# Optimization experiments

Hardware: AMD Instinct MI355X
Metric: run time of the kernel (lower is better)

## Reference

```python
import jax, jax.numpy as jnp
import numpy as np

N, E = 40000, 640000
EMB, HID, H, TXT = 128, 128, 4, 384
C = HID // H  # per-head channels = 32


def _prelu(x, a):
    return jnp.where(x >= 0, x, a * x)


def _layernorm(x, g, b, eps=1e-5):
    m = jnp.mean(x, axis=-1, keepdims=True)
    v = jnp.mean((x - m) ** 2, axis=-1, keepdims=True)
    return (x - m) / jnp.sqrt(v + eps) * g + b


def _gat_conv(h, src, dst, W, att_src, att_dst, bias):
    # PyG GATConv (concat=True, eval mode): lin has no bias, self-loops already in src/dst.
    xh = (h @ W.T).reshape(N, H, C)                      # [N,H,C]
    a_src = jnp.sum(xh * att_src, axis=-1)               # [N,H]
    a_dst = jnp.sum(xh * att_dst, axis=-1)               # [N,H]
    alpha = jax.nn.leaky_relu(a_src[src] + a_dst[dst], negative_slope=0.2)  # [Et,H]
    amax = jax.ops.segment_max(alpha, dst, num_segments=N)
    ex = jnp.exp(alpha - amax[dst])
    denom = jax.ops.segment_sum(ex, dst, num_segments=N)
    coef = ex / denom[dst]                               # scatter-softmax over dst
    out = jax.ops.segment_sum(xh[src] * coef[:, :, None], dst, num_segments=N)
    return out.reshape(N, H * C) + bias


def setup_inputs() -> dict:
    key = jax.random.key(0)
    ks = jax.random.split(key, 20)
    nrm = lambda k, s, sc=0.05: jax.random.normal(k, s, jnp.float32) * sc
    inp = {
        "x": nrm(ks[0], (N, EMB), 1.0),
        "num_x": nrm(ks[1], (N, 1), 1.0),
        "num_mask": jnp.ones((N,), jnp.float32),
        "txt_x": nrm(ks[2], (N, TXT), 1.0),
        "txt_mask": jnp.ones((N,), jnp.float32),
        "edge_index": jax.random.randint(ks[3], (2, E), 0, N, jnp.int32),
        "num_proj_w": nrm(ks[4], (EMB, 1)), "num_proj_b": jnp.zeros((EMB,), jnp.float32),
        "txt_proj_w": nrm(ks[5], (EMB, TXT)), "txt_proj_b": jnp.zeros((EMB,), jnp.float32),
        "node_proj_w": nrm(ks[6], (HID, EMB)), "node_proj_b": jnp.zeros((HID,), jnp.float32),
        "prelu0_a": jnp.full((HID,), 0.25, jnp.float32),
        "conv1_w": nrm(ks[7], (HID, HID)), "att_src1": nrm(ks[8], (H, C)), "att_dst1": nrm(ks[9], (H, C)), "bias1": jnp.zeros((HID,), jnp.float32),
        "norm1_g": jnp.ones((HID,), jnp.float32), "norm1_b": jnp.zeros((HID,), jnp.float32),
        "prelu1_a": jnp.full((HID,), 0.25, jnp.float32),
        "conv2_w": nrm(ks[10], (HID, HID)), "att_src2": nrm(ks[11], (H, C)), "att_dst2": nrm(ks[12], (H, C)), "bias2": jnp.zeros((HID,), jnp.float32),
        "norm2_g": jnp.ones((HID,), jnp.float32), "norm2_b": jnp.zeros((HID,), jnp.float32),
        "prelu2_a": jnp.full((HID,), 0.25, jnp.float32),
        "out_w": nrm(ks[13], (1, HID)), "out_b": jnp.zeros((1,), jnp.float32),
    }
    return inp


def reference(x, num_x, num_mask, txt_x, txt_mask, edge_index,
              num_proj_w, num_proj_b, txt_proj_w, txt_proj_b,
              node_proj_w, node_proj_b, prelu0_a,
              conv1_w, att_src1, att_dst1, bias1, norm1_g, norm1_b, prelu1_a,
              conv2_w, att_src2, att_dst2, bias2, norm2_g, norm2_b, prelu2_a,
              out_w, out_b):
    # add self loops (PyG GATConv default)
    loop = jnp.arange(N, dtype=edge_index.dtype)
    src = jnp.concatenate([edge_index[0], loop])
    dst = jnp.concatenate([edge_index[1], loop])

    h = (num_x * num_mask[:, None]) @ num_proj_w.T + num_proj_b
    h = h + (txt_x * txt_mask[:, None]) @ txt_proj_w.T + txt_proj_b
    h = h + x @ node_proj_w.T + node_proj_b
    h = _prelu(h, prelu0_a)

    h = _gat_conv(h, src, dst, conv1_w, att_src1, att_dst1, bias1)
    h = _prelu(_layernorm(h, norm1_g, norm1_b), prelu1_a)  # dropout: eval mode -> identity

    h = _gat_conv(h, src, dst, conv2_w, att_src2, att_dst2, bias2)
    h = _prelu(_layernorm(h, norm2_g, norm2_b), prelu2_a)

    return (h @ out_w.T + out_b).squeeze(-1)  # [N]
```

## Files before the change

### kernel.cpp

```cpp
#include <hip/hip_runtime.h>
#include <stdint.h>

typedef unsigned short u16;
typedef unsigned int u32;
typedef __attribute__((ext_vector_type(8))) short bf16x8;
typedef __attribute__((ext_vector_type(4))) float f32x4;

__device__ __forceinline__ float bf2f(u32 u) {
    union { u32 i; float f; } v; v.i = u << 16; return v.f;
}
__device__ __forceinline__ u16 f2bf(float f) {
    u32 x = __float_as_uint(f);
    return (u16)((x + 0x7fffu + ((x >> 16) & 1u)) >> 16);
}
__device__ __forceinline__ float wred_sum(float v) {
#pragma unroll
    for (int o = 32; o > 0; o >>= 1) v += __shfl_xor(v, o, 64);
    return v;
}
__device__ __forceinline__ bf16x8 ldA_f32(const float* p, size_t off) {
    union { uint4 u; bf16x8 b; } t;
    const float* af = p + off;
    float4 a = *(const float4*)af, b2 = *(const float4*)(af + 4);
    t.u.x = (u32)f2bf(a.x)  | ((u32)f2bf(a.y)  << 16);
    t.u.y = (u32)f2bf(a.z)  | ((u32)f2bf(a.w)  << 16);
    t.u.z = (u32)f2bf(b2.x) | ((u32)f2bf(b2.y) << 16);
    t.u.w = (u32)f2bf(b2.z) | ((u32)f2bf(b2.w) << 16);
    return t.b;
}
__device__ __forceinline__ bf16x8 ld16B(const u16* p, size_t off) {
    union { uint4 u; bf16x8 b; } t; t.u = *(const uint4*)(p + off); return t.b;
}
__device__ __forceinline__ bf16x8 ldB(const u16* sw, int ct, int ks, int l16, int quad) {
    union { uint4 u; bf16x8 b; } t;
    t.u = *(const uint4*)&sw[(ct * 16 + l16) * 136 + ks * 32 + quad * 8];
    return t.b;
}
__device__ __forceinline__ void stage256_f32(const float* W, int stride, int koff,
                                             u16* sw, int tid) {
#pragma unroll
    for (int it = 0; it < 8; ++it) {
        int idx = (it * 256 + tid) * 8;
        int c = idx >> 7, kk = idx & 127;
        const float* wf = W + (size_t)c * stride + koff + kk;
        float4 a = *(const float4*)wf, b = *(const float4*)(wf + 4);
        uint4 v;
        v.x = (u32)f2bf(a.x) | ((u32)f2bf(a.y) << 16);
        v.y = (u32)f2bf(a.z) | ((u32)f2bf(a.w) << 16);
        v.z = (u32)f2bf(b.x) | ((u32)f2bf(b.y) << 16);
        v.w = (u32)f2bf(b.z) | ((u32)f2bf(b.w) << 16);
        *(uint4*)&sw[c * 136 + kk] = v;
    }
}

__global__ void k_zero(int* __restrict__ p, int n) {
    int i = blockIdx.x * 256 + threadIdx.x;
    if (i < n) p[i] = 0;
}
__global__ void k_hist(const int* __restrict__ dst, int E, int* __restrict__ deg) {
    int e = blockIdx.x * 256 + threadIdx.x;
    if (e < E) atomicAdd(&deg[dst[e]], 1);
}
__global__ __launch_bounds__(1024) void k_scanA(const int* __restrict__ deg, int n,
                                                int* __restrict__ out, int* __restrict__ bsum) {
    __shared__ int wsum[16];
    int t = threadIdx.x, w = t >> 6, lane = t & 63;
    int i0 = blockIdx.x * 4096 + t * 4;
    int4 v = make_int4(0, 0, 0, 0);
    if (i0 + 3 < n) v = *(const int4*)&deg[i0];
    else {
        if (i0 < n)     v.x = deg[i0];
        if (i0 + 1 < n) v.y = deg[i0 + 1];
        if (i0 + 2 < n) v.z = deg[i0 + 2];
    }
    int tsum = v.x + v.y + v.z + v.w;
    int s = tsum;
#pragma unroll
    for (int o = 1; o < 64; o <<= 1) { int u = __shfl_up(s, o, 64); if (lane >= o) s += u; }
    if (lane == 63) wsum[w] = s;
    __syncthreads();
    if (w == 0 && lane < 16) {
        int ws = wsum[lane];
#pragma unroll
        for (int o = 1; o < 16; o <<= 1) { int u = __shfl_up(ws, o, 64); if (lane >= o) ws += u; }
        wsum[lane] = ws;
    }
    __syncthreads();
    int woff = (w == 0) ? 0 : wsum[w - 1];
    int p = woff + s - tsum;
    if (i0 + 3 < n) {
        int4 o4; o4.x = p; o4.y = p + v.x; o4.z = p + v.x + v.y; o4.w = p + v.x + v.y + v.z;
        *(int4*)&out[i0] = o4;
    } else {
        int pp = p;
        if (i0 < n)     { out[i0] = pp;     pp += v.x; }
        if (i0 + 1 < n) { out[i0 + 1] = pp; pp += v.y; }
        if (i0 + 2 < n) { out[i0 + 2] = pp; }
    }
    if (t == 0) bsum[blockIdx.x] = wsum[15];
}
__global__ void k_scanB(int* __restrict__ bsum, int nb, int* __restrict__ total) {
    int lane = threadIdx.x;
    int v = (lane < nb) ? bsum[lane] : 0;
    int s = v;
#pragma unroll
    for (int o = 1; o < 64; o <<= 1) { int u = __shfl_up(s, o, 64); if (lane >= o) s += u; }
    if (lane < nb) bsum[lane] = s - v;
    if (lane == 63) total[0] = s;
}
__global__ void k_scanC(int* __restrict__ rowptr, int* __restrict__ cursor,
                        const int* __restrict__ boff, int n) {
    int i = blockIdx.x * 256 + threadIdx.x;
    if (i < n) {
        int r = rowptr[i] + boff[i >> 12];
        rowptr[i] = r; cursor[i] = r;
    }
}
__global__ void k_scatter(const int* __restrict__ srcp, const int* __restrict__ dstp, int E,
                          int* __restrict__ cursor, int* __restrict__ col) {
    int e = blockIdx.x * 256 + threadIdx.x;
    if (e < E) {
        int p = atomicAdd(&cursor[dstp[e]], 1);
        col[p] = srcp[e];
    }
}

__global__ __launch_bounds__(256) void k_fused1(
    const float* __restrict__ x, const float* __restrict__ numx, const float* __restrict__ numm,
    const float* __restrict__ txt, const float* __restrict__ txtm,
    const float* __restrict__ numw, const float* __restrict__ numb,
    const float* __restrict__ txtw, const float* __restrict__ txtb,
    const float* __restrict__ nodew, const float* __restrict__ nodeb,
    const float* __restrict__ pa,
    const float* __restrict__ W1, const float* __restrict__ atts, const float* __restrict__ attd,
    u16* __restrict__ xh, float* __restrict__ asrc, float* __restrict__ adst) {
    __shared__ u16 sw[128 * 136];
    __shared__ u16 sh[4][16 * 136];
    int tid = threadIdx.x, w = tid >> 6, lane = tid & 63, quad = lane >> 4, l16 = lane & 15;
    int nb = blockIdx.x * 64 + w * 16;
    f32x4 acc[8];
#pragma unroll
    for (int ct = 0; ct < 8; ++ct) { f32x4 z = {0.f, 0.f, 0.f, 0.f}; acc[ct] = z; }

    for (int chunk = 0; chunk < 3; ++chunk) {
        __syncthreads();
        stage256_f32(txtw, 384, chunk * 128, sw, tid);
        __syncthreads();
#pragma unroll
        for (int ks = 0; ks < 4; ++ks) {
            bf16x8 a0 = ldA_f32(txt, (size_t)(nb + l16) * 384 + chunk * 128 + ks * 32 + quad * 8);
#pragma unroll
            for (int ct = 0; ct < 8; ++ct)
                acc[ct] = __builtin_amdgcn_mfma_f32_16x16x32_bf16(
                    a0, ldB(sw, ct, ks, l16, quad), acc[ct], 0, 0, 0);
        }
    }
#pragma unroll
    for (int r = 0; r < 4; ++r) {
        float tm = txtm[nb + quad * 4 + r];
#pragma unroll
        for (int ct = 0; ct < 8; ++ct) acc[ct][r] *= tm;
    }
    __syncthreads();
    stage256_f32(nodew, 128, 0, sw, tid);
    __syncthreads();
#pragma unroll
    for (int ks = 0; ks < 4; ++ks) {
        bf16x8 a0 = ldA_f32(x, (size_t)(nb + l16) * 128 + ks * 32 + quad * 8);
#pragma unroll
        for (int ct = 0; ct < 8; ++ct)
            acc[ct] = __builtin_amdgcn_mfma_f32_16x16x32_bf16(
                a0, ldB(sw, ct, ks, l16, quad), acc[ct], 0, 0, 0);
    }
    float nm[4];
#pragma unroll
    for (int r = 0; r < 4; ++r) {
        int n = nb + quad * 4 + r;
        nm[r] = numx[n] * numm[n];
    }
#pragma unroll
    for (int ct = 0; ct < 8; ++ct) {
        int c = ct * 16 + l16;
        float cw = numw[c];
        float cb = numb[c] + txtb[c] + nodeb[c];
        float pav = pa[c];
#pragma unroll
        for (int r = 0; r < 4; ++r) {
            float v = acc[ct][r] + nm[r] * cw + cb;
            v = v >= 0.f ? v : pav * v;
            sh[w][(quad * 4 + r) * 136 + c] = f2bf(v);
        }
    }
    __syncthreads();
    stage256_f32(W1, 128, 0, sw, tid);
    __syncthreads();
    f32x4 a2[8];
#pragma unroll
    for (int ct = 0; ct < 8; ++ct) { f32x4 z = {0.f, 0.f, 0.f, 0.f}; a2[ct] = z; }
#pragma unroll
    for (int ks = 0; ks < 4; ++ks) {
        bf16x8 a0 = ld16B(sh[w], l16 * 136 + ks * 32 + quad * 8);
#pragma unroll
        for (int ct = 0; ct < 8; ++ct)
            a2[ct] = __builtin_amdgcn_mfma_f32_16x16x32_bf16(
                a0, ldB(sw, ct, ks, l16, quad), a2[ct], 0, 0, 0);
    }
#pragma unroll
    for (int ct = 0; ct < 8; ++ct) {
        int c = ct * 16 + l16;
#pragma unroll
        for (int r = 0; r < 4; ++r)
            xh[(size_t)(nb + quad * 4 + r) * 128 + c] = f2bf(a2[ct][r]);
    }
    float as_[8], ad_[8];
#pragma unroll
    for (int ct = 0; ct < 8; ++ct) {
        int c = ct * 16 + l16;
        as_[ct] = atts[c];
        ad_[ct] = attd[c];
    }
#pragma unroll
    for (int hh = 0; hh < 4; ++hh) {
        float vs[4], vd[4];
#pragma unroll
        for (int r = 0; r < 4; ++r) {
            vs[r] = a2[2 * hh][r] * as_[2 * hh] + a2[2 * hh + 1][r] * as_[2 * hh + 1];
            vd[r] = a2[2 * hh][r] * ad_[2 * hh] + a2[2 * hh + 1][r] * ad_[2 * hh + 1];
        }
#pragma unroll
        for (int o = 1; o <= 8; o <<= 1) {
#pragma unroll
            for (int r = 0; r < 4; ++r) {
                vs[r] += __shfl_xor(vs[r], o, 64);
                vd[r] += __shfl_xor(vd[r], o, 64);
            }
        }
        if ((l16 >> 2) == hh) {
            int r = l16 & 3;
            float ss = (r == 0) ? vs[0] : (r == 1) ? vs[1] : (r == 2) ? vs[2] : vs[3];
            float dd = (r == 0) ? vd[0] : (r == 1) ? vd[1] : (r == 2) ? vd[2] : vd[3];
            int n = nb + quad * 4 + r;
            asrc[n * 4 + hh] = ss;
            adst[n * 4 + hh] = dd;
        }
    }
}

__global__ __launch_bounds__(256) void k_xh(
    const u16* __restrict__ h, const float* __restrict__ W,
    const float* __restrict__ att_s, const float* __restrict__ att_d,
    u16* __restrict__ xh, float* __restrict__ asrc, float* __restrict__ adst) {
    __shared__ u16 sw[128 * 136];
    int tid = threadIdx.x;
    int w = tid >> 6, lane = tid & 63, quad = lane >> 4, l16 = lane & 15;
    int nb = blockIdx.x * 64 + w * 16;
    f32x4 acc[8];
#pragma unroll
    for (int ct = 0; ct < 8; ++ct) { f32x4 z = {0.f, 0.f, 0.f, 0.f}; acc[ct] = z; }

    stage256_f32(W, 128, 0, sw, tid);
    __syncthreads();
#pragma unroll
    for (int ks = 0; ks < 4; ++ks) {
        bf16x8 a0 = ld16B(h, (size_t)(nb + l16) * 128 + ks * 32 + quad * 8);
#pragma unroll
        for (int ct = 0; ct < 8; ++ct)
            acc[ct] = __builtin_amdgcn_mfma_f32_16x16x32_bf16(
                a0, ldB(sw, ct, ks, l16, quad), acc[ct], 0, 0, 0);
    }
#pragma unroll
    for (int ct = 0; ct < 8; ++ct) {
        int c = ct * 16 + l16;
#pragma unroll
        for (int r = 0; r < 4; ++r) {
            int n = nb + quad * 4 + r;
            xh[(size_t)n * 128 + c] = f2bf(acc[ct][r]);
        }
    }
    float as_[8], ad_[8];
#pragma unroll
    for (int ct = 0; ct < 8; ++ct) {
        int c = ct * 16 + l16;
        as_[ct] = att_s[c];
        ad_[ct] = att_d[c];
    }
#pragma unroll
    for (int hh = 0; hh < 4; ++hh) {
        float vs[4], vd[4];
#pragma unroll
        for (int r = 0; r < 4; ++r) {
            vs[r] = acc[2 * hh][r] * as_[2 * hh] + acc[2 * hh + 1][r] * as_[2 * hh + 1];
            vd[r] = acc[2 * hh][r] * ad_[2 * hh] + acc[2 * hh + 1][r] * ad_[2 * hh + 1];
        }
#pragma unroll
        for (int o = 1; o <= 8; o <<= 1) {
#pragma unroll
            for (int r = 0; r < 4; ++r) {
                vs[r] += __shfl_xor(vs[r], o, 64);
                vd[r] += __shfl_xor(vd[r], o, 64);
            }
        }
        if ((l16 >> 2) == hh) {
            int r = l16 & 3;
            float ss = (r == 0) ? vs[0] : (r == 1) ? vs[1] : (r == 2) ? vs[2] : vs[3];
            float dd = (r == 0) ? vd[0] : (r == 1) ? vd[1] : (r == 2) ? vd[2] : vd[3];
            int n = nb + quad * 4 + r;
            asrc[n * 4 + hh] = ss;
            adst[n * 4 + hh] = dd;
        }
    }
}

__global__ __launch_bounds__(64) void k_agg(
    const u16* __restrict__ xh, const float* __restrict__ asrc, const float* __restrict__ adst,
    const int* __restrict__ rowptr, const int* __restrict__ col,
    const float* __restrict__ bias, const float* __restrict__ g, const float* __restrict__ b,
    const float* __restrict__ pa, u16* __restrict__ hnext,
    const float* __restrict__ outw, const float* __restrict__ outb, float* __restrict__ outy,
    int is_final) {
    __shared__ int   scol[64];
    __shared__ float scoef[64][4];
    int n = blockIdx.x, lane = threadIdx.x;
    int beg = rowptr[n], end = rowptr[n + 1];
    const float4* asrc4 = (const float4*)asrc;

    float4 adv = ((const float4*)adst)[n];
    float ad[4] = { adv.x, adv.y, adv.z, adv.w };
    float4 asv = asrc4[n];
    float els[4];
#pragma unroll
    for (int h = 0; h < 4; h++) {
        float a = ((const float*)&asv)[h] + ad[h];
        a = a >= 0.f ? a : 0.2f * a;
        els[h] = __expf(a);
    }
    int hh = lane >> 4;
    u32 vself = ((const u32*)(xh + (size_t)n * 128))[lane];
    float acc0 = els[hh] * bf2f(vself & 0xffffu);
    float acc1 = els[hh] * bf2f(vself >> 16);
    float a0b = 0.f, a1b = 0.f, a0c = 0.f, a1c = 0.f, a0d = 0.f, a1d = 0.f;
    float l[4] = { 0.f, 0.f, 0.f, 0.f };

    for (int base = beg; base < end; base += 64) {
        int e = base + lane;
        int cnt = min(64, end - base);
        if (e < end) {
            int s = col[e];
            float4 av = asrc4[s];
            scol[lane] = s;
            float cf[4];
#pragma unroll
            for (int h = 0; h < 4; h++) {
                float a = ((const float*)&av)[h] + ad[h];
                a = a >= 0.f ? a : 0.2f * a;
                cf[h] = __expf(a);
                l[h] += cf[h];
            }
            *(float4*)scoef[lane] = make_float4(cf[0], cf[1], cf[2], cf[3]);
        }
        __syncthreads();
        int j = 0;
        for (; j + 3 < cnt; j += 4) {
            int s0 = scol[j], s1 = scol[j + 1], s2 = scol[j + 2], s3 = scol[j + 3];
            float c0 = scoef[j][hh], c1 = scoef[j + 1][hh];
            float c2 = scoef[j + 2][hh], c3 = scoef[j + 3][hh];
            u32 v0 = ((const u32*)(xh + (size_t)s0 * 128))[lane];
            u32 v1 = ((const u32*)(xh + (size_t)s1 * 128))[lane];
            u32 v2 = ((const u32*)(xh + (size_t)s2 * 128))[lane];
            u32 v3 = ((const u32*)(xh + (size_t)s3 * 128))[lane];
            acc0 += c0 * bf2f(v0 & 0xffffu);  acc1 += c0 * bf2f(v0 >> 16);
            a0b  += c1 * bf2f(v1 & 0xffffu);  a1b  += c1 * bf2f(v1 >> 16);
            a0c  += c2 * bf2f(v2 & 0xffffu);  a1c  += c2 * bf2f(v2 >> 16);
            a0d  += c3 * bf2f(v3 & 0xffffu);  a1d  += c3 * bf2f(v3 >> 16);
        }
        for (; j < cnt; ++j) {
            int s0 = scol[j];
            float c0 = scoef[j][hh];
            u32 v0 = ((const u32*)(xh + (size_t)s0 * 128))[lane];
            acc0 += c0 * bf2f(v0 & 0xffffu);
            acc1 += c0 * bf2f(v0 >> 16);
        }
        __syncthreads();
    }
    acc0 += a0b + a0c + a0d;
    acc1 += a1b + a1c + a1d;

    float L[4];
#pragma unroll
    for (int h = 0; h < 4; h++) L[h] = wred_sum(l[h]) + els[h];
    float inv = 1.f / L[hh];
    acc0 *= inv;
    acc1 *= inv;

    int c0i = 2 * lane;
    float2 bi = *(const float2*)(bias + c0i);
    acc0 += bi.x; acc1 += bi.y;

    float mean = wred_sum(acc0 + acc1) * (1.f / 128.f);
    float d0 = acc0 - mean, d1 = acc1 - mean;
    float var = wred_sum(d0 * d0 + d1 * d1) * (1.f / 128.f);
    float rstd = rsqrtf(var + 1e-5f);
    float2 gg = *(const float2*)(g + c0i);
    float2 bb = *(const float2*)(b + c0i);
    float2 pp = *(const float2*)(pa + c0i);
    float y0 = d0 * rstd * gg.x + bb.x;
    float y1 = d1 * rstd * gg.y + bb.y;
    y0 = y0 >= 0.f ? y0 : pp.x * y0;
    y1 = y1 >= 0.f ? y1 : pp.y * y1;

    if (is_final) {
        float2 ow = *(const float2*)(outw + c0i);
        float dot = wred_sum(y0 * ow.x + y1 * ow.y);
        if (lane == 0) outy[n] = dot + outb[0];
    } else {
        ((u32*)(hnext + (size_t)n * 128))[lane] = (u32)f2bf(y0) | ((u32)f2bf(y1) << 16);
    }
}

extern "C" void kernel_launch(void* const* d_in, const int* in_sizes, int n_in,
                              void* d_out, int out_size, void* d_ws, size_t ws_size,
                              hipStream_t stream) {
    const int N = in_sizes[2];
    const int E = in_sizes[5] / 2;

    const float* x      = (const float*)d_in[0];
    const float* numx   = (const float*)d_in[1];
    const float* numm   = (const float*)d_in[2];
    const float* txt    = (const float*)d_in[3];
    const float* txtm   = (const float*)d_in[4];
    const int*   ei     = (const int*)d_in[5];
    const float* numw   = (const float*)d_in[6];
    const float* numb   = (const float*)d_in[7];
    const float* txtw   = (const float*)d_in[8];
    const float* txtb   = (const float*)d_in[9];
    const float* nodew  = (const float*)d_in[10];
    const float* nodeb  = (const float*)d_in[11];
    const float* pa0    = (const float*)d_in[12];
    const float* conv1w = (const float*)d_in[13];
    const float* atts1  = (const float*)d_in[14];
    const float* attd1  = (const float*)d_in[15];
    const float* bias1  = (const float*)d_in[16];
    const float* g1     = (const float*)d_in[17];
    const float* b1     = (const float*)d_in[18];
    const float* pa1    = (const float*)d_in[19];
    const float* conv2w = (const float*)d_in[20];
    const float* atts2  = (const float*)d_in[21];
    const float* attd2  = (const float*)d_in[22];
    const float* bias2  = (const float*)d_in[23];
    const float* g2     = (const float*)d_in[24];
    const float* b2     = (const float*)d_in[25];
    const float* pa2    = (const float*)d_in[26];
    const float* outw   = (const float*)d_in[27];
    const float* outb   = (const float*)d_in[28];

    const int* srcp = ei;
    const int* dstp = ei + E;

    char* p = (char*)d_ws;
    auto alloc = [&](size_t bytes) -> void* {
        void* q = (void*)p;
        p += (bytes + 255) & ~(size_t)255;
        return q;
    };
    u16*   hA     = (u16*)alloc((size_t)N * 128 * 2);
    u16*   hB     = (u16*)alloc((size_t)N * 128 * 2);
    float* asrc   = (float*)alloc((size_t)N * 4 * 4);
    float* adst   = (float*)alloc((size_t)N * 4 * 4);
    int*   deg    = (int*)alloc((size_t)N * 4);
    int*   rowptr = (int*)alloc((size_t)(N + 1) * 4);
    int*   cursor = (int*)alloc((size_t)N * 4);
    int*   col    = (int*)alloc((size_t)E * 4);
    int*   bsum   = (int*)alloc(64 * 4);

    const int nbScan = (N + 4095) / 4096;
    k_zero<<<(N + 255) / 256, 256, 0, stream>>>(deg, N);
    k_hist<<<(E + 255) / 256, 256, 0, stream>>>(dstp, E, deg);
    k_scanA<<<nbScan, 1024, 0, stream>>>(deg, N, rowptr, bsum);
    k_scanB<<<1, 64, 0, stream>>>(bsum, nbScan, rowptr + N);
    k_scanC<<<(N + 255) / 256, 256, 0, stream>>>(rowptr, cursor, bsum, N);
    k_scatter<<<(E + 255) / 256, 256, 0, stream>>>(srcp, dstp, E, cursor, col);

    const int gProj = N / 64;

    k_fused1<<<gProj, 256, 0, stream>>>(x, numx, numm, txt, txtm, numw, numb,
                                        txtw, txtb, nodew, nodeb, pa0,
                                        conv1w, atts1, attd1, hB, asrc, adst);
    k_agg<<<N, 64, 0, stream>>>(hB, asrc, adst, rowptr, col, bias1, g1, b1, pa1,
                                hA, nullptr, nullptr, nullptr, 0);

    k_xh<<<gProj, 256, 0, stream>>>(hA, conv2w, atts2, attd2, hB, asrc, adst);
    k_agg<<<N, 64, 0, stream>>>(hB, asrc, adst, rowptr, col, bias2, g2, b2, pa2,
                                nullptr, outw, outb, (float*)d_out, 1);
}
```

Before: 330.4 us.

## Pack four nodes per aggregation block, unroll gathers by eight, vectorize CSR build

The aggregation kernel now processes four destination nodes per 256-thread block, one wavefront each, with per-wave shared buffers. This removes the block-wide barriers, since each wave only reads its own staging area. The gather loop is unrolled to eight outstanding row loads to raise memory-level parallelism. Histogram and scatter kernels now read four edge indices per thread with int4 loads, which cuts the thread count. Dropping the barriers relies on wave-level execution ordering for the shared-memory writes and reads, with no explicit fence.

Measured after the change: 331.8 us. Within noise of the previous version (+0.4%).

```diff
diff --git a/kernel.cpp b/kernel.cpp
--- a/kernel.cpp
+++ b/kernel.cpp
@@ -58,8 +58,16 @@
     if (i < n) p[i] = 0;
 }
 __global__ void k_hist(const int* __restrict__ dst, int E, int* __restrict__ deg) {
-    int e = blockIdx.x * 256 + threadIdx.x;
-    if (e < E) atomicAdd(&deg[dst[e]], 1);
+    int i0 = (blockIdx.x * 256 + threadIdx.x) * 4;
+    if (i0 + 3 < E) {
+        int4 d = *(const int4*)&dst[i0];
+        atomicAdd(&deg[d.x], 1);
+        atomicAdd(&deg[d.y], 1);
+        atomicAdd(&deg[d.z], 1);
+        atomicAdd(&deg[d.w], 1);
+    } else {
+        for (int e = i0; e < E; ++e) atomicAdd(&deg[dst[e]], 1);
+    }
 }
 __global__ __launch_bounds__(1024) void k_scanA(const int* __restrict__ deg, int n,
                                                 int* __restrict__ out, int* __restrict__ bsum) {
@@ -118,10 +126,17 @@
 }
 __global__ void k_scatter(const int* __restrict__ srcp, const int* __restrict__ dstp, int E,
                           int* __restrict__ cursor, int* __restrict__ col) {
-    int e = blockIdx.x * 256 + threadIdx.x;
-    if (e < E) {
-        int p = atomicAdd(&cursor[dstp[e]], 1);
-        col[p] = srcp[e];
+    int i0 = (blockIdx.x * 256 + threadIdx.x) * 4;
+    if (i0 + 3 < E) {
+        int4 s = *(const int4*)&srcp[i0];
+        int4 d = *(const int4*)&dstp[i0];
+        col[atomicAdd(&cursor[d.x], 1)] = s.x;
+        col[atomicAdd(&cursor[d.y], 1)] = s.y;
+        col[atomicAdd(&cursor[d.z], 1)] = s.z;
+        col[atomicAdd(&cursor[d.w], 1)] = s.w;
+    } else {
+        for (int e = i0; e < E; ++e)
+            col[atomicAdd(&cursor[dstp[e]], 1)] = srcp[e];
     }
 }
 
@@ -311,16 +326,18 @@
     }
 }
 
-__global__ __launch_bounds__(64) void k_agg(
+__global__ __launch_bounds__(256) void k_agg(
     const u16* __restrict__ xh, const float* __restrict__ asrc, const float* __restrict__ adst,
     const int* __restrict__ rowptr, const int* __restrict__ col,
     const float* __restrict__ bias, const float* __restrict__ g, const float* __restrict__ b,
     const float* __restrict__ pa, u16* __restrict__ hnext,
     const float* __restrict__ outw, const float* __restrict__ outb, float* __restrict__ outy,
-    int is_final) {
-    __shared__ int   scol[64];
-    __shared__ float scoef[64][4];
-    int n = blockIdx.x, lane = threadIdx.x;
+    int is_final, int N) {
+    __shared__ int   scol[4][64];
+    __shared__ float scoef[4][64][4];
+    int tid = threadIdx.x, w = tid >> 6, lane = tid & 63;
+    int n = blockIdx.x * 4 + w;
+    if (n >= N) return;
     int beg = rowptr[n], end = rowptr[n + 1];
     const float4* asrc4 = (const float4*)asrc;
 
@@ -347,7 +364,7 @@
         if (e < end) {
             int s = col[e];
             float4 av = asrc4[s];
-            scol[lane] = s;
+            scol[w][lane] = s;
             float cf[4];
 #pragma unroll
             for (int h = 0; h < 4; h++) {
@@ -356,31 +373,50 @@
                 cf[h] = __expf(a);
                 l[h] += cf[h];
             }
-            *(float4*)scoef[lane] = make_float4(cf[0], cf[1], cf[2], cf[3]);
-        }
-        __syncthreads();
+            *(float4*)scoef[w][lane] = make_float4(cf[0], cf[1], cf[2], cf[3]);
+        }
         int j = 0;
-        for (; j + 3 < cnt; j += 4) {
-            int s0 = scol[j], s1 = scol[j + 1], s2 = scol[j + 2], s3 = scol[j + 3];
-            float c0 = scoef[j][hh], c1 = scoef[j + 1][hh];
-            float c2 = scoef[j + 2][hh], c3 = scoef[j + 3][hh];
+        for (; j + 7 < cnt; j += 8) {
+            int s0 = scol[w][j],     s1 = scol[w][j + 1];
+            int s2 = scol[w][j + 2], s3 = scol[w][j + 3];
+            int s4 = scol[w][j + 4], s5 = scol[w][j + 5];
+            int s6 = scol[w][j + 6], s7 = scol[w][j + 7];
             u32 v0 = ((const u32*)(xh + (size_t)s0 * 128))[lane];
             u32 v1 = ((const u32*)(xh + (size_t)s1 * 128))[lane];
             u32 v2 = ((const u32*)(xh + (size_t)s2 * 128))[lane];
             u32 v3 = ((const u32*)(xh + (size_t)s3 * 128))[lane];
+            u32 v4 = ((const u32*)(xh + (size_t)s4 * 128))[lane];
+            u32 v5 = ((const u32*)(xh + (size_t)s5 * 128))[lane];
+            u32 v6 = ((const u32*)(xh + (size_t)s6 * 128))[lane];
+            u32 v7 = ((const u32*)(xh + (size_t)s7 * 128))[lane];
+            float c0 = scoef[w][j][hh],     c1 = scoef[w][j + 1][hh];
+            float c2 = scoef[w][j + 2][hh], c3 = scoef[w][j + 3][hh];
+            float c4 = scoef[w][j + 4][hh], c5 = scoef[w][j + 5][hh];
+            float c6 = scoef[w][j + 6][hh], c7 = scoef[w][j + 7][hh];
             acc0 += c0 * bf2f(v0 & 0xffffu);  acc1 += c0 * bf2f(v0 >> 16);
             a0b  += c1 * bf2f(v1 & 0xffffu);  a1b  += c1 * bf2f(v1 >> 16);
             a0c  += c2 * bf2f(v2 & 0xffffu);  a1c  += c2 * bf2f(v2 >> 16);
             a0d  += c3 * bf2f(v3 & 0xffffu);  a1d  += c3 * bf2f(v3 >> 16);
-        }
-        for (; j < cnt; ++j) {
-            int s0 = scol[j];
-            float c0 = scoef[j][hh];
+            acc0 += c4 * bf2f(v4 & 0xffffu);  acc1 += c4 * bf2f(v4 >> 16);
+            a0b  += c5 * bf2f(v5 & 0xffffu);  a1b  += c5 * bf2f(v5 >> 16);
+            a0c  += c6 * bf2f(v6 & 0xffffu);  a1c  += c6 * bf2f(v6 >> 16);
+            a0d  += c7 * bf2f(v7 & 0xffffu);  a1d  += c7 * bf2f(v7 >> 16);
+        }
+        for (; j + 1 < cnt; j += 2) {
+            int s0 = scol[w][j], s1 = scol[w][j + 1];
+            u32 v0 = ((const u32*)(xh + (size_t)s0 * 128))[lane];
+            u32 v1 = ((const u32*)(xh + (size_t)s1 * 128))[lane];
+            float c0 = scoef[w][j][hh], c1 = scoef[w][j + 1][hh];
+            acc0 += c0 * bf2f(v0 & 0xffffu);  acc1 += c0 * bf2f(v0 >> 16);
+            a0b  += c1 * bf2f(v1 & 0xffffu);  a1b  += c1 * bf2f(v1 >> 16);
+        }
+        if (j < cnt) {
+            int s0 = scol[w][j];
+            float c0 = scoef[w][j][hh];
             u32 v0 = ((const u32*)(xh + (size_t)s0 * 128))[lane];
             acc0 += c0 * bf2f(v0 & 0xffffu);
             acc1 += c0 * bf2f(v0 >> 16);
         }
-        __syncthreads();
     }
     acc0 += a0b + a0c + a0d;
     acc1 += a1b + a1c + a1d;
@@ -474,21 +510,22 @@
 
     const int nbScan = (N + 4095) / 4096;
     k_zero<<<(N + 255) / 256, 256, 0, stream>>>(deg, N);
-    k_hist<<<(E + 255) / 256, 256, 0, stream>>>(dstp, E, deg);
+    k_hist<<<(E / 4 + 255) / 256, 256, 0, stream>>>(dstp, E, deg);
     k_scanA<<<nbScan, 1024, 0, stream>>>(deg, N, rowptr, bsum);
     k_scanB<<<1, 64, 0, stream>>>(bsum, nbScan, rowptr + N);
     k_scanC<<<(N + 255) / 256, 256, 0, stream>>>(rowptr, cursor, bsum, N);
-    k_scatter<<<(E + 255) / 256, 256, 0, stream>>>(srcp, dstp, E, cursor, col);
+    k_scatter<<<(E / 4 + 255) / 256, 256, 0, stream>>>(srcp, dstp, E, cursor, col);
 
     const int gProj = N / 64;
+    const int gAgg  = (N + 3) / 4;
 
     k_fused1<<<gProj, 256, 0, stream>>>(x, numx, numm, txt, txtm, numw, numb,
                                         txtw, txtb, nodew, nodeb, pa0,
                                         conv1w, atts1, attd1, hB, asrc, adst);
-    k_agg<<<N, 64, 0, stream>>>(hB, asrc, adst, rowptr, col, bias1, g1, b1, pa1,
-                                hA, nullptr, nullptr, nullptr, 0);
+    k_agg<<<gAgg, 256, 0, stream>>>(hB, asrc, adst, rowptr, col, bias1, g1, b1, pa1,
+                                    hA, nullptr, nullptr, nullptr, 0, N);
 
     k_xh<<<gProj, 256, 0, stream>>>(hA, conv2w, atts2, attd2, hB, asrc, adst);
-    k_agg<<<N, 64, 0, stream>>>(hB, asrc, adst, rowptr, col, bias2, g2, b2, pa2,
-                                nullptr, outw, outb, (float*)d_out, 1);
-}
+    k_agg<<<gAgg, 256, 0, stream>>>(hB, asrc, adst, rowptr, col, bias2, g2, b2, pa2,
+                                    nullptr, outw, outb, (float*)d_out, 1, N);
+}
```
